# Kernel optimization log

Hardware: AMD Instinct MI355X
Metric: run time of the kernel (lower is better)

The kernel has to match this reference:

```python
import jax, jax.numpy as jnp
import numpy as np

HIDDEN = 1024
HEADS = 16
HEAD_DIM = HIDDEN // HEADS  # 64
RP_DIM = 256
KERNEL_EPS = 1e-3


def _gaussian_orthogonal_matrix(nb_rows, nb_cols, seed=0):
    """Orthogonal random features (scaling=0), as in Performer FAVOR+."""
    rng = np.random.RandomState(seed)
    blocks = []
    n_full = nb_rows // nb_cols
    for _ in range(n_full):
        q, _ = np.linalg.qr(rng.randn(nb_cols, nb_cols))
        blocks.append(q.T)
    rem = nb_rows - n_full * nb_cols
    if rem > 0:
        q, _ = np.linalg.qr(rng.randn(nb_cols, nb_cols))
        blocks.append(q.T[:rem])
    mat = np.concatenate(blocks, axis=0)
    # scaling=0: row norms drawn from chi distribution (norms of gaussian rows)
    multiplier = np.linalg.norm(rng.randn(nb_rows, nb_cols), axis=1)
    return (multiplier[:, None] * mat).astype(np.float32)


def setup_inputs() -> dict:
    key = jax.random.key(0)
    kx, kw = jax.random.split(key)
    x = jax.random.normal(kx, (4, 4096, HIDDEN), dtype=jnp.float32)
    w_qkv = jax.random.normal(kw, (HIDDEN, 3 * HIDDEN), dtype=jnp.float32) * 0.02
    b_qkv = jnp.zeros((3 * HIDDEN,), dtype=jnp.float32)
    proj = jnp.asarray(_gaussian_orthogonal_matrix(RP_DIM, HEAD_DIM))  # [M, Dh]
    return {"x": x, "w_qkv": w_qkv, "b_qkv": b_qkv, "proj": proj}


def reference(x, w_qkv, b_qkv, proj):
    B, N, _ = x.shape
    qkv = x @ w_qkv + b_qkv  # [B, N, 3*hidden]
    q, k, v = jnp.split(qkv, 3, axis=-1)

    def to_heads(t):
        return t.reshape(B, N, HEADS, HEAD_DIM).transpose(0, 2, 1, 3)  # bhnd

    q, k, v = to_heads(q), to_heads(k), to_heads(v)

    # forward scales by d**-0.25, generalized_kernel normalizes by d**-0.25 again
    scale = HEAD_DIM ** -0.5
    # generalized kernel features: relu(x_norm @ proj^T) + eps  -> [B,H,N,M]
    q_prime = jax.nn.relu(jnp.einsum('bhnd,md->bhnm', q * scale, proj)) + KERNEL_EPS
    k_prime = jax.nn.relu(jnp.einsum('bhnd,md->bhnm', k * scale, proj)) + KERNEL_EPS

    # non-causal linear attention
    k_sum = k_prime.sum(axis=2)  # [B,H,M]
    d_inv = 1.0 / jnp.einsum('bhnm,bhm->bhn', q_prime, k_sum)  # [B,H,N]
    context = jnp.einsum('bhnm,bhnd->bhmd', k_prime, v)  # [B,H,M,Dh]
    out = jnp.einsum('bhmd,bhnm,bhn->bhnd', context, q_prime, d_inv)

    out = out.transpose(0, 2, 1, 3).reshape(B, N, HIDDEN)
    return out
```

## Files before the change

### kernel.cpp

```cpp
#include <hip/hip_runtime.h>

#define B_   4
#define N_   4096
#define NH   16
#define DH   64
#define HID  1024
#define NC3  3072
#define M_   256
#define BH   64
#define SCALE 0.125f
#define EPS   1e-3f
#define CH2  8
#define CH3  16

typedef _Float16 half8  __attribute__((ext_vector_type(8)));
typedef _Float16 half4v __attribute__((ext_vector_type(4)));
typedef float floatx4   __attribute__((ext_vector_type(4)));

#define GLD_LDS16(gptr, lds_base) \
  __builtin_amdgcn_global_load_lds((const __attribute__((address_space(1))) void*)(gptr), \
                                   (__attribute__((address_space(3))) void*)(lds_base), 16, 0, 0)

#define SBAR() asm volatile("s_barrier" ::: "memory")

__global__ __launch_bounds__(256) void convert_xh(
    const float* __restrict__ x, _Float16* __restrict__ xh)
{
    const size_t i = ((size_t)blockIdx.x * 256 + threadIdx.x) * 8;
    float4 a = *(const float4*)(x + i);
    float4 b = *(const float4*)(x + i + 4);
    half8 h;
    h[0] = (_Float16)a.x; h[1] = (_Float16)a.y; h[2] = (_Float16)a.z; h[3] = (_Float16)a.w;
    h[4] = (_Float16)b.x; h[5] = (_Float16)b.y; h[6] = (_Float16)b.z; h[7] = (_Float16)b.w;
    *(half8*)(xh + i) = h;
}

__global__ __launch_bounds__(256) void convert_wT(
    const float* __restrict__ w, _Float16* __restrict__ wT)
{
    __shared__ float t[64][65];
    const int tid = threadIdx.x;
    const int kb = blockIdx.y * 64, nb = blockIdx.x * 64;
    const int c = tid & 63, r0 = tid >> 6;
#pragma unroll
    for (int rr = 0; rr < 64; rr += 4)
        t[rr + r0][c] = w[(size_t)(kb + rr + r0) * NC3 + nb + c];
    __syncthreads();
    const float sc = (nb < 2048) ? SCALE : 1.0f;
#pragma unroll
    for (int rr = 0; rr < 64; rr += 4)
        wT[(size_t)(nb + rr + r0) * HID + kb + c] = (_Float16)(t[c][rr + r0] * sc);
}

__global__ __launch_bounds__(256) void convert_projh(
    const float* __restrict__ proj, _Float16* __restrict__ projh)
{
    const int i = blockIdx.x * 256 + threadIdx.x;
    projh[i] = (_Float16)proj[i];
}

__device__ __forceinline__ void stage_tile_qkv(
    const _Float16* __restrict__ xh, const _Float16* __restrict__ wT,
    int row0, int col0, int kt, char* ab, char* bb, int wv, int srow, int sblk)
{
    const size_t ko = (size_t)kt * 64;
#pragma unroll
    for (int s = 0; s < 4; ++s) {
        const int r = s * 64 + srow;
        GLD_LDS16(xh + (size_t)(row0 + r) * HID + ko + 8 * sblk, ab + s * 8192 + wv * 1024);
        GLD_LDS16(wT + (size_t)(col0 + r) * HID + ko + 8 * sblk, bb + s * 8192 + wv * 1024);
    }
}

__global__ __launch_bounds__(512, 2) void gemm_qkv_mfma(
    const _Float16* __restrict__ xh, const _Float16* __restrict__ wT,
    const float* __restrict__ bias,
    _Float16* __restrict__ qh, _Float16* __restrict__ kh, _Float16* __restrict__ vTh)
{
    __shared__ __align__(16) char smem[131072];

    const int tid  = threadIdx.x;
    const int lane = tid & 63;
    const int wv   = tid >> 6;
    const int wm   = wv >> 2;
    const int wn   = wv & 3;
    const int lr   = lane & 15;
    const int lg   = lane >> 4;
    const int lr7  = lr & 7;

    const int bid  = blockIdx.x;
    const int tile = ((bid & 7) * 96) + (bid >> 3);
    const int tm   = tile / 12;
    const int tn   = tile - tm * 12;
    const int row0 = tm * 256;
    const int col0 = tn * 256;

    const int srow = 8 * wv + (lane >> 3);
    const int sblk = (lane & 7) ^ (lane >> 3);

    char* buf0A = smem;
    char* buf0B = smem + 32768;
    char* buf1A = smem + 65536;
    char* buf1B = smem + 98304;

    floatx4 acc[8][4] = {};

    stage_tile_qkv(xh, wT, row0, col0, 0, buf0A, buf0B, wv, srow, sblk);
    stage_tile_qkv(xh, wT, row0, col0, 1, buf1A, buf1B, wv, srow, sblk);

    for (int t = 0; t < 16; ++t) {
        if (t < 15) asm volatile("s_waitcnt vmcnt(8)" ::: "memory");
        else        asm volatile("s_waitcnt vmcnt(0)" ::: "memory");
        SBAR();

        char* ab = (t & 1) ? buf1A : buf0A;
        char* bb = (t & 1) ? buf1B : buf0B;

        half8 a0[8], b0[4];
#pragma unroll
        for (int i = 0; i < 8; ++i)
            a0[i] = *(const half8*)(ab + (wm * 128 + 16 * i + lr) * 128 + ((lg ^ lr7) * 16));
#pragma unroll
        for (int j = 0; j < 4; ++j)
            b0[j] = *(const half8*)(bb + (wn * 64 + 16 * j + lr) * 128 + ((lg ^ lr7) * 16));

        __builtin_amdgcn_s_setprio(1);
#pragma unroll
        for (int i = 0; i < 8; ++i)
#pragma unroll
            for (int j = 0; j < 4; ++j)
                acc[i][j] = __builtin_amdgcn_mfma_f32_16x16x32_f16(a0[i], b0[j], acc[i][j], 0, 0, 0);
        __builtin_amdgcn_s_setprio(0);

        half8 a1[8], b1[4];
#pragma unroll
        for (int i = 0; i < 8; ++i)
            a1[i] = *(const half8*)(ab + (wm * 128 + 16 * i + lr) * 128 + (((4 + lg) ^ lr7) * 16));
#pragma unroll
        for (int j = 0; j < 4; ++j)
            b1[j] = *(const half8*)(bb + (wn * 64 + 16 * j + lr) * 128 + (((4 + lg) ^ lr7) * 16));

        asm volatile("s_waitcnt lgkmcnt(0)" ::: "memory");
        SBAR();
        if (t < 14)
            stage_tile_qkv(xh, wT, row0, col0, t + 2, ab, bb, wv, srow, sblk);

        __builtin_amdgcn_s_setprio(1);
#pragma unroll
        for (int i = 0; i < 8; ++i)
#pragma unroll
            for (int j = 0; j < 4; ++j)
                acc[i][j] = __builtin_amdgcn_mfma_f32_16x16x32_f16(a1[i], b1[j], acc[i][j], 0, 0, 0);
        __builtin_amdgcn_s_setprio(0);
    }

#pragma unroll
    for (int j = 0; j < 4; ++j) {
        const int col = col0 + wn * 64 + 16 * j + lr;
        const int which = col >> 10;
        const int h = (col >> 6) & 15;
        const int d = col & 63;
        const float bb2 = bias[col] * ((which < 2) ? SCALE : 1.0f);
        if (which == 2) {
#pragma unroll
            for (int i = 0; i < 8; ++i) {
                const int m0 = row0 + wm * 128 + 16 * i + 4 * lg;
                const int bi = m0 >> 12, n0 = m0 & (N_ - 1);
                half4v hv;
#pragma unroll
                for (int rg = 0; rg < 4; ++rg) hv[rg] = (_Float16)(acc[i][j][rg] + bb2);
                *(half4v*)(vTh + ((size_t)(bi * NH + h) * DH + d) * N_ + n0) = hv;
            }
        } else {
            _Float16* dst = (which == 0) ? qh : kh;
#pragma unroll
            for (int i = 0; i < 8; ++i)
#pragma unroll
                for (int rg = 0; rg < 4; ++rg) {
                    const int m = row0 + wm * 128 + 16 * i + 4 * lg + rg;
                    const int bi = m >> 12, n = m & (N_ - 1);
                    dst[((size_t)(bi * NH + h) * N_ + n) * DH + d] =
                        (_Float16)(acc[i][j][rg] + bb2);
                }
        }
    }
}

__global__ __launch_bounds__(256) void kv_ctx_mfma(
    const _Float16* __restrict__ kh, const _Float16* __restrict__ vTh,
    const _Float16* __restrict__ projh,
    float* __restrict__ ctx_part, float* __restrict__ ksum_part)
{
    __shared__ __align__(16) _Float16 Kt[64 * 64];
    __shared__ __align__(16) _Float16 Vt[64 * 64];
    __shared__ __align__(16) _Float16 Sp[256 * 64];

    const int tid  = threadIdx.x;
    const int lane = tid & 63;
    const int wv   = tid >> 6;
    const int lr = lane & 15, lg = lane >> 4;
    const int bh = blockIdx.y, chunk = blockIdx.x;
    const int n_base = chunk * (N_ / CH2);

    half8 bfP[4][2];
#pragma unroll
    for (int j = 0; j < 4; ++j)
#pragma unroll
        for (int ks = 0; ks < 2; ++ks)
            bfP[j][ks] = *(const half8*)(projh + (size_t)(64 * wv + 16 * j + lr) * DH + 32 * ks + 8 * lg);

    floatx4 cacc[4][4] = {};
    float ks_acc[4] = {0.f, 0.f, 0.f, 0.f};

    for (int t = 0; t < (N_ / CH2) / 64; ++t) {
        const int n0 = n_base + t * 64;
        __syncthreads();
#pragma unroll
        for (int s = 0; s < 2; ++s) {
            const int R = wv * 16 + s * 8;
            const int r = R + (lane >> 3);
            const int db = (lane & 7) ^ (r & 7);
            GLD_LDS16(kh + ((size_t)(bh * N_ + n0 + r)) * DH + db * 8, (char*)Kt + R * 128);
        }
#pragma unroll
        for (int s = 0; s < 2; ++s) {
            const int R = wv * 16 + s * 8;
            const int r = R + (lane >> 3);
            const int db = (lane & 7) ^ (r & 7);
            GLD_LDS16(vTh + ((size_t)(bh * DH + r)) * N_ + n0 + db * 8, (char*)Vt + R * 128);
        }
        __syncthreads();

        floatx4 s[4][4] = {};
#pragma unroll
        for (int ks = 0; ks < 2; ++ks) {
            half8 aK[4];
#pragma unroll
            for (int i = 0; i < 4; ++i) {
                const int r = 16 * i + lr;
                aK[i] = *(const half8*)((const char*)Kt + r * 128 + (((4 * ks + lg) ^ (r & 7)) * 16));
            }
#pragma unroll
            for (int i = 0; i < 4; ++i)
#pragma unroll
                for (int j = 0; j < 4; ++j)
                    s[i][j] = __builtin_amdgcn_mfma_f32_16x16x32_f16(aK[i], bfP[j][ks], s[i][j], 0, 0, 0);
        }
#pragma unroll
        for (int i = 0; i < 4; ++i)
#pragma unroll
            for (int j = 0; j < 4; ++j) {
                const int m = 64 * wv + 16 * j + lr;
                const int nn0 = 16 * i + 4 * lg;
                half4v h4;
#pragma unroll
                for (int rg = 0; rg < 4; ++rg) {
                    const float kv = fmaxf(s[i][j][rg], 0.f) + EPS;
                    ks_acc[j] += kv;
                    h4[rg] = (_Float16)kv;
                }
                const int db = nn0 >> 3, sub = nn0 & 7;
                *(half4v*)((char*)Sp + m * 128 + ((db ^ (m & 7)) * 16) + sub * 2) = h4;
            }
#pragma unroll
        for (int ks = 0; ks < 2; ++ks) {
            half8 aV[4], bS[4];
#pragma unroll
            for (int i = 0; i < 4; ++i) {
                const int r = 16 * i + lr;
                aV[i] = *(const half8*)((const char*)Vt + r * 128 + (((4 * ks + lg) ^ (r & 7)) * 16));
            }
#pragma unroll
            for (int j = 0; j < 4; ++j) {
                const int m = 64 * wv + 16 * j + lr;
                bS[j] = *(const half8*)((const char*)Sp + m * 128 + (((4 * ks + lg) ^ (m & 7)) * 16));
            }
#pragma unroll
            for (int i = 0; i < 4; ++i)
#pragma unroll
                for (int j = 0; j < 4; ++j)
                    cacc[i][j] = __builtin_amdgcn_mfma_f32_16x16x32_f16(aV[i], bS[j], cacc[i][j], 0, 0, 0);
        }
    }

#pragma unroll
    for (int i = 0; i < 4; ++i)
#pragma unroll
        for (int j = 0; j < 4; ++j)
#pragma unroll
            for (int rg = 0; rg < 4; ++rg) {
                const int d = 16 * i + 4 * lg + rg;
                const int m = 64 * wv + 16 * j + lr;
                ctx_part[(((size_t)chunk * BH + bh) * DH + d) * M_ + m] = cacc[i][j][rg];
            }
#pragma unroll
    for (int j = 0; j < 4; ++j) {
        float v = ks_acc[j];
        v += __shfl_xor(v, 16);
        v += __shfl_xor(v, 32);
        if (lg == 0)
            ksum_part[((size_t)chunk * BH + bh) * M_ + 64 * wv + 16 * j + lr] = v;
    }
}

__global__ __launch_bounds__(256) void reduce_ctx(
    const float* __restrict__ ctx_part, const float* __restrict__ ksum_part,
    _Float16* __restrict__ ctxTh, _Float16* __restrict__ ksumh)
{
    const int idx = blockIdx.x * 256 + threadIdx.x;
    const int CTX = BH * DH * M_;
    if (idx < CTX) {
        float sum = 0.f;
#pragma unroll
        for (int c = 0; c < CH2; ++c) sum += ctx_part[(size_t)c * CTX + idx];
        ctxTh[idx] = (_Float16)sum;
    } else {
        const int kidx = idx - CTX;
        if (kidx < BH * M_) {
            float sum = 0.f;
#pragma unroll
            for (int c = 0; c < CH2; ++c) sum += ksum_part[(size_t)c * BH * M_ + kidx];
            ksumh[kidx] = (_Float16)sum;
        }
    }
}

__global__ __launch_bounds__(256) void attn_out_mfma(
    const _Float16* __restrict__ qh, const _Float16* __restrict__ projh,
    const _Float16* __restrict__ ctxTh, const _Float16* __restrict__ ksumh,
    float* __restrict__ out)
{
    __shared__ __align__(16) _Float16 Sp[64 * 256];

    const int tid  = threadIdx.x;
    const int lane = tid & 63;
    const int wv   = tid >> 6;
    const int lr = lane & 15, lg = lane >> 4;
    const int bh = blockIdx.y;
    const int bi = bh >> 4, h = bh & 15;
    const int n_base = blockIdx.x * (N_ / CH3);

    half8 afP[4][2];
#pragma unroll
    for (int I = 0; I < 4; ++I)
#pragma unroll
        for (int ks = 0; ks < 2; ++ks)
            afP[I][ks] = *(const half8*)(projh + (size_t)(64 * wv + 16 * I + lr) * DH + 32 * ks + 8 * lg);

    for (int t = 0; t < (N_ / CH3) / 64; ++t) {
        const int n0 = n_base + t * 64;
        __syncthreads();
        floatx4 sacc[4][4] = {};
#pragma unroll
        for (int ks = 0; ks < 2; ++ks) {
            half8 bq[4];
#pragma unroll
            for (int J = 0; J < 4; ++J)
                bq[J] = *(const half8*)(qh + ((size_t)bh * N_ + n0 + 16 * J + lr) * DH + 32 * ks + 8 * lg);
#pragma unroll
            for (int I = 0; I < 4; ++I)
#pragma unroll
                for (int J = 0; J < 4; ++J)
                    sacc[I][J] = __builtin_amdgcn_mfma_f32_16x16x32_f16(afP[I][ks], bq[J], sacc[I][J], 0, 0, 0);
        }
#pragma unroll
        for (int I = 0; I < 4; ++I)
#pragma unroll
            for (int J = 0; J < 4; ++J) {
                const int n = 16 * J + lr;
                const int m0 = 64 * wv + 16 * I + 4 * lg;
                half4v h4;
#pragma unroll
                for (int rg = 0; rg < 4; ++rg)
                    h4[rg] = (_Float16)(fmaxf(sacc[I][J][rg], 0.f) + EPS);
                const int db = m0 >> 3, sub = m0 & 7;
                *(half4v*)((char*)Sp + n * 512 + ((db ^ (n & 31)) * 16) + sub * 2) = h4;
            }
        __syncthreads();
        floatx4 oacc[4] = {};
        floatx4 dacc = {};
        const int nl = 16 * wv + lr;
#pragma unroll
        for (int ks = 0; ks < 8; ++ks) {
            half8 aq = *(const half8*)((const char*)Sp + nl * 512 + (((4 * ks + lg) ^ (nl & 31)) * 16));
#pragma unroll
            for (int j = 0; j < 4; ++j) {
                half8 bc = *(const half8*)(ctxTh + ((size_t)bh * DH + 16 * j + lr) * M_ + 32 * ks + 8 * lg);
                oacc[j] = __builtin_amdgcn_mfma_f32_16x16x32_f16(aq, bc, oacc[j], 0, 0, 0);
            }
            half8 bk = {};
            if (lr == 0)
                bk = *(const half8*)(ksumh + (size_t)bh * M_ + 32 * ks + 8 * lg);
            dacc = __builtin_amdgcn_mfma_f32_16x16x32_f16(aq, bk, dacc, 0, 0, 0);
        }
#pragma unroll
        for (int rg = 0; rg < 4; ++rg) {
            float den = dacc[rg];
            den = __shfl(den, lane & 48);
            const float dinv = 1.f / den;
            const int n = n0 + 16 * wv + 4 * lg + rg;
#pragma unroll
            for (int j = 0; j < 4; ++j)
                out[(((size_t)bi * N_ + n) * NH + h) * DH + 16 * j + lr] = oacc[j][rg] * dinv;
        }
    }
}

extern "C" void kernel_launch(void* const* d_in, const int* in_sizes, int n_in,
                              void* d_out, int out_size, void* d_ws, size_t ws_size,
                              hipStream_t stream) {
    const float* x    = (const float*)d_in[0];
    const float* w    = (const float*)d_in[1];
    const float* bias = (const float*)d_in[2];
    const float* proj = (const float*)d_in[3];
    float* out = (float*)d_out;
    char* ws = (char*)d_ws;

    const size_t XN  = (size_t)B_ * N_ * HID;
    const size_t QKV = (size_t)BH * N_ * DH;
    const size_t CTX = (size_t)BH * DH * M_;

    _Float16* xh       = (_Float16*)ws;                          ws += XN * 2;
    _Float16* wT       = (_Float16*)ws;                          ws += NC3 * HID * 2;
    _Float16* projh    = (_Float16*)ws;                          ws += M_ * DH * 2;
    _Float16* qh       = (_Float16*)ws;                          ws += QKV * 2;
    _Float16* kh       = (_Float16*)ws;                          ws += QKV * 2;
    _Float16* vTh      = (_Float16*)ws;                          ws += QKV * 2;
    _Float16* ctxTh    = (_Float16*)ws;                          ws += CTX * 2;
    _Float16* ksumh    = (_Float16*)ws;                          ws += BH * M_ * 2;
    float*    ctx_part = (float*)ws;                             ws += (size_t)CH2 * CTX * 4;
    float*    ksum_part= (float*)ws;                             ws += (size_t)CH2 * BH * M_ * 4;

    convert_xh<<<dim3(XN / (256 * 8)), 256, 0, stream>>>(x, xh);
    convert_wT<<<dim3(NC3 / 64, HID / 64), 256, 0, stream>>>(w, wT);
    convert_projh<<<dim3(M_ * DH / 256), 256, 0, stream>>>(proj, projh);

    gemm_qkv_mfma<<<dim3(768), dim3(512), 0, stream>>>(xh, wT, bias, qh, kh, vTh);

    kv_ctx_mfma<<<dim3(CH2, BH), 256, 0, stream>>>(kh, vTh, projh, ctx_part, ksum_part);

    reduce_ctx<<<dim3((CTX + BH * M_ + 255) / 256), 256, 0, stream>>>(ctx_part, ksum_part, ctxTh, ksumh);

    attn_out_mfma<<<dim3(CH3, BH), 256, 0, stream>>>(qh, projh, ctxTh, ksumh, out);
}
```

Before: 359.5 us.

## Restructure QKV GEMM into 4-stage K=32 pipeline with interleaved staging

Replaces the double-buffered K=64 tile loop in the QKV projection GEMM with a four-buffer ring of K=32 slices, prefetching three slices ahead. Global-to-LDS loads are split into halves and interleaved between the two MFMA phases, and the LDS swizzle changes to match the 64-byte rows. The aim is to hide global-load latency more deeply and cut register pressure, since B fragments are reused across both phases. The cost is twice as many loop iterations and more barriers per unit of work.

```diff
diff --git a/kernel.cpp b/kernel.cpp
--- a/kernel.cpp
+++ b/kernel.cpp
@@ -59,19 +59,6 @@
     projh[i] = (_Float16)proj[i];
 }
 
-__device__ __forceinline__ void stage_tile_qkv(
-    const _Float16* __restrict__ xh, const _Float16* __restrict__ wT,
-    int row0, int col0, int kt, char* ab, char* bb, int wv, int srow, int sblk)
-{
-    const size_t ko = (size_t)kt * 64;
-#pragma unroll
-    for (int s = 0; s < 4; ++s) {
-        const int r = s * 64 + srow;
-        GLD_LDS16(xh + (size_t)(row0 + r) * HID + ko + 8 * sblk, ab + s * 8192 + wv * 1024);
-        GLD_LDS16(wT + (size_t)(col0 + r) * HID + ko + 8 * sblk, bb + s * 8192 + wv * 1024);
-    }
-}
-
 __global__ __launch_bounds__(512, 2) void gemm_qkv_mfma(
     const _Float16* __restrict__ xh, const _Float16* __restrict__ wT,
     const float* __restrict__ bias,
@@ -86,7 +73,6 @@
     const int wn   = wv & 3;
     const int lr   = lane & 15;
     const int lg   = lane >> 4;
-    const int lr7  = lr & 7;
 
     const int bid  = blockIdx.x;
     const int tile = ((bid & 7) * 96) + (bid >> 3);
@@ -95,62 +81,81 @@
     const int row0 = tm * 256;
     const int col0 = tn * 256;
 
-    const int srow = 8 * wv + (lane >> 3);
-    const int sblk = (lane & 7) ^ (lane >> 3);
-
-    char* buf0A = smem;
-    char* buf0B = smem + 32768;
-    char* buf1A = smem + 65536;
-    char* buf1B = smem + 98304;
+    const int sr0 = (wv * 2) * 16 + (lane >> 2);
+    const int sdb = (lane & 3) ^ ((lane >> 3) & 3);
+    const _Float16* gA0 = xh + (size_t)(row0 + sr0) * HID + 8 * sdb;
+    const _Float16* gA1 = gA0 + (size_t)16 * HID;
+    const _Float16* gB0 = wT + (size_t)(col0 + sr0) * HID + 8 * sdb;
+    const _Float16* gB1 = gB0 + (size_t)16 * HID;
+    const int offS0 = (wv * 2) * 1024;
+    const int offS1 = offS0 + 1024;
+
+    const int po   = (lg ^ ((lr >> 1) & 3)) * 16;
+    const int aoff = (wm * 128 + lr) * 64 + po;
+    const int boff = (wn * 64 + lr) * 64 + po;
 
     floatx4 acc[8][4] = {};
 
-    stage_tile_qkv(xh, wT, row0, col0, 0, buf0A, buf0B, wv, srow, sblk);
-    stage_tile_qkv(xh, wT, row0, col0, 1, buf1A, buf1B, wv, srow, sblk);
-
-    for (int t = 0; t < 16; ++t) {
-        if (t < 15) asm volatile("s_waitcnt vmcnt(8)" ::: "memory");
-        else        asm volatile("s_waitcnt vmcnt(0)" ::: "memory");
+#pragma unroll
+    for (int pt = 0; pt < 3; ++pt) {
+        char* ab = smem + pt * 32768;
+        char* bb = ab + 16384;
+        const int k0 = pt * 32;
+        GLD_LDS16(gA0 + k0, ab + offS0);
+        GLD_LDS16(gB0 + k0, bb + offS0);
+        GLD_LDS16(gA1 + k0, ab + offS1);
+        GLD_LDS16(gB1 + k0, bb + offS1);
+    }
+
+    for (int t = 0; t < 32; ++t) {
+        if (t < 30)      asm volatile("s_waitcnt vmcnt(8)" ::: "memory");
+        else if (t == 30) asm volatile("s_waitcnt vmcnt(4)" ::: "memory");
+        else             asm volatile("s_waitcnt vmcnt(0)" ::: "memory");
         SBAR();
 
-        char* ab = (t & 1) ? buf1A : buf0A;
-        char* bb = (t & 1) ? buf1B : buf0B;
-
-        half8 a0[8], b0[4];
-#pragma unroll
-        for (int i = 0; i < 8; ++i)
-            a0[i] = *(const half8*)(ab + (wm * 128 + 16 * i + lr) * 128 + ((lg ^ lr7) * 16));
+        char* ab  = smem + (t & 3) * 32768;
+        char* bb  = ab + 16384;
+        char* sab = smem + ((t + 3) & 3) * 32768;
+        char* sbb = sab + 16384;
+        const int ks = (t + 3) * 32;
+        const bool do_stage = (t <= 28);
+
+        half8 b0[4], a0[4];
 #pragma unroll
         for (int j = 0; j < 4; ++j)
-            b0[j] = *(const half8*)(bb + (wn * 64 + 16 * j + lr) * 128 + ((lg ^ lr7) * 16));
-
+            b0[j] = *(const half8*)(bb + boff + j * 1024);
+#pragma unroll
+        for (int i = 0; i < 4; ++i)
+            a0[i] = *(const half8*)(ab + aoff + i * 1024);
+        if (do_stage) {
+            GLD_LDS16(gA0 + ks, sab + offS0);
+            GLD_LDS16(gB0 + ks, sbb + offS0);
+        }
+        SBAR();
         __builtin_amdgcn_s_setprio(1);
 #pragma unroll
-        for (int i = 0; i < 8; ++i)
+        for (int i = 0; i < 4; ++i)
 #pragma unroll
             for (int j = 0; j < 4; ++j)
                 acc[i][j] = __builtin_amdgcn_mfma_f32_16x16x32_f16(a0[i], b0[j], acc[i][j], 0, 0, 0);
         __builtin_amdgcn_s_setprio(0);
-
-        half8 a1[8], b1[4];
-#pragma unroll
-        for (int i = 0; i < 8; ++i)
-            a1[i] = *(const half8*)(ab + (wm * 128 + 16 * i + lr) * 128 + (((4 + lg) ^ lr7) * 16));
-#pragma unroll
-        for (int j = 0; j < 4; ++j)
-            b1[j] = *(const half8*)(bb + (wn * 64 + 16 * j + lr) * 128 + (((4 + lg) ^ lr7) * 16));
-
-        asm volatile("s_waitcnt lgkmcnt(0)" ::: "memory");
         SBAR();
-        if (t < 14)
-            stage_tile_qkv(xh, wT, row0, col0, t + 2, ab, bb, wv, srow, sblk);
-
+
+        half8 a1[4];
+#pragma unroll
+        for (int i = 0; i < 4; ++i)
+            a1[i] = *(const half8*)(ab + aoff + (4 + i) * 1024);
+        if (do_stage) {
+            GLD_LDS16(gA1 + ks, sab + offS1);
+            GLD_LDS16(gB1 + ks, sbb + offS1);
+        }
+        SBAR();
         __builtin_amdgcn_s_setprio(1);
 #pragma unroll
-        for (int i = 0; i < 8; ++i)
+        for (int i = 0; i < 4; ++i)
 #pragma unroll
             for (int j = 0; j < 4; ++j)
-                acc[i][j] = __builtin_amdgcn_mfma_f32_16x16x32_f16(a1[i], b1[j], acc[i][j], 0, 0, 0);
+                acc[4 + i][j] = __builtin_amdgcn_mfma_f32_16x16x32_f16(a1[i], b0[j], acc[4 + i][j], 0, 0, 0);
         __builtin_amdgcn_s_setprio(0);
     }
 
```

Result: no change. 365.0 us (+1.5%).

## Double-buffer K/V LDS tiles in kv_ctx_mfma to overlap loads with MFMA

Applied to the files above, without the earlier changes.

Splits the K and V shared-memory tiles into two buffers. The global-to-LDS loads for the next 64-row tile are issued before the current tile is computed, instead of loading and waiting on every iteration. One of the two barriers per iteration is removed and global addresses are precomputed outside the loop. This doubles K/V LDS usage, which may reduce occupancy, and relies on the loop-top barrier waiting for the outstanding LDS DMA.

```diff
diff --git a/kernel.cpp b/kernel.cpp
--- a/kernel.cpp
+++ b/kernel.cpp
@@ -191,8 +191,8 @@
     const _Float16* __restrict__ projh,
     float* __restrict__ ctx_part, float* __restrict__ ksum_part)
 {
-    __shared__ __align__(16) _Float16 Kt[64 * 64];
-    __shared__ __align__(16) _Float16 Vt[64 * 64];
+    __shared__ __align__(16) _Float16 Kt[2][64 * 64];
+    __shared__ __align__(16) _Float16 Vt[2][64 * 64];
     __shared__ __align__(16) _Float16 Sp[256 * 64];
 
     const int tid  = threadIdx.x;
@@ -201,6 +201,13 @@
     const int lr = lane & 15, lg = lane >> 4;
     const int bh = blockIdx.y, chunk = blockIdx.x;
     const int n_base = chunk * (N_ / CH2);
+    const int NT = (N_ / CH2) / 64;
+
+    const int srw = lane >> 3;
+    const int sdb = (lane & 7) ^ srw;
+    const _Float16* gK = kh  + ((size_t)bh * N_ + wv * 16 + srw) * DH + sdb * 8;
+    const _Float16* gV = vTh + ((size_t)bh * DH + wv * 16 + srw) * N_ + sdb * 8;
+    const int ldsR0 = (wv * 16) * 128;
 
     half8 bfP[4][2];
 #pragma unroll
@@ -212,24 +219,26 @@
     floatx4 cacc[4][4] = {};
     float ks_acc[4] = {0.f, 0.f, 0.f, 0.f};
 
-    for (int t = 0; t < (N_ / CH2) / 64; ++t) {
-        const int n0 = n_base + t * 64;
+    {
+        const size_t n0 = n_base;
+        GLD_LDS16(gK + n0 * DH,             (char*)Kt[0] + ldsR0);
+        GLD_LDS16(gK + (n0 + 8) * DH,       (char*)Kt[0] + ldsR0 + 8 * 128);
+        GLD_LDS16(gV + n0,                  (char*)Vt[0] + ldsR0);
+        GLD_LDS16(gV + n0 + 8 * (size_t)N_, (char*)Vt[0] + ldsR0 + 8 * 128);
+    }
+
+    for (int t = 0; t < NT; ++t) {
         __syncthreads();
-#pragma unroll
-        for (int s = 0; s < 2; ++s) {
-            const int R = wv * 16 + s * 8;
-            const int r = R + (lane >> 3);
-            const int db = (lane & 7) ^ (r & 7);
-            GLD_LDS16(kh + ((size_t)(bh * N_ + n0 + r)) * DH + db * 8, (char*)Kt + R * 128);
-        }
-#pragma unroll
-        for (int s = 0; s < 2; ++s) {
-            const int R = wv * 16 + s * 8;
-            const int r = R + (lane >> 3);
-            const int db = (lane & 7) ^ (r & 7);
-            GLD_LDS16(vTh + ((size_t)(bh * DH + r)) * N_ + n0 + db * 8, (char*)Vt + R * 128);
-        }
-        __syncthreads();
+        if (t + 1 < NT) {
+            const size_t n1 = n_base + (size_t)(t + 1) * 64;
+            const int b = (t + 1) & 1;
+            GLD_LDS16(gK + n1 * DH,             (char*)Kt[b] + ldsR0);
+            GLD_LDS16(gK + (n1 + 8) * DH,       (char*)Kt[b] + ldsR0 + 8 * 128);
+            GLD_LDS16(gV + n1,                  (char*)Vt[b] + ldsR0);
+            GLD_LDS16(gV + n1 + 8 * (size_t)N_, (char*)Vt[b] + ldsR0 + 8 * 128);
+        }
+        const _Float16* KtB = Kt[t & 1];
+        const _Float16* VtB = Vt[t & 1];
 
         floatx4 s[4][4] = {};
 #pragma unroll
@@ -238,7 +247,7 @@
 #pragma unroll
             for (int i = 0; i < 4; ++i) {
                 const int r = 16 * i + lr;
-                aK[i] = *(const half8*)((const char*)Kt + r * 128 + (((4 * ks + lg) ^ (r & 7)) * 16));
+                aK[i] = *(const half8*)((const char*)KtB + r * 128 + (((4 * ks + lg) ^ (r & 7)) * 16));
             }
 #pragma unroll
             for (int i = 0; i < 4; ++i)
@@ -268,7 +277,7 @@
 #pragma unroll
             for (int i = 0; i < 4; ++i) {
                 const int r = 16 * i + lr;
-                aV[i] = *(const half8*)((const char*)Vt + r * 128 + (((4 * ks + lg) ^ (r & 7)) * 16));
+                aV[i] = *(const half8*)((const char*)VtB + r * 128 + (((4 * ks + lg) ^ (r & 7)) * 16));
             }
 #pragma unroll
             for (int j = 0; j < 4; ++j) {
```

After: 372.4 us. 3.6% more time.
